# Performance work log

Hardware: AMD Instinct MI355X
Metric: run time of the kernel (lower is better)

The kernel has to match this reference:

```python
import jax, jax.numpy as jnp
import numpy as np

N_NODES = 100000
N_EDGES = 3200000
WINDOW = 200


def setup_inputs() -> dict:
    key = jax.random.key(0)
    k1, k2, k3, k4, k5 = jax.random.split(key, 5)
    loss_series = jax.random.normal(k1, (N_NODES, WINDOW), dtype=jnp.float32)
    W_series = jax.random.normal(k2, (1, WINDOW), dtype=jnp.float32) / WINDOW
    W_graph = jax.random.normal(k3, (1, 2), dtype=jnp.float32) * 0.1
    edge_src = jax.random.randint(k4, (N_EDGES,), 0, N_NODES, dtype=jnp.int32)
    edge_dst = jax.random.randint(k5, (N_EDGES,), 0, N_NODES, dtype=jnp.int32)
    return {
        "loss_series": loss_series,
        "W_series": W_series,
        "W_graph": W_graph,
        "edge_src": edge_src,
        "edge_dst": edge_dst,
    }


def reference(loss_series, W_series, W_graph, edge_src, edge_dst):
    # series aggregation: Linear(window_size -> 1, no bias)  -> h: [N, 1]
    h = loss_series @ W_series.T
    n = loss_series.shape[0]
    neg_inf = jnp.float32(-jnp.inf)

    # remove self-loops: neutralize their messages for the max-reduce
    self_loop = (edge_src == edge_dst)[:, None]

    # forward graph: copy_u('feat') then max over incoming edges per dst
    msg_fwd = jnp.where(self_loop, neg_inf, h[edge_src])        # [E, 1]
    pre_feat = jax.ops.segment_max(msg_fwd, edge_dst, num_segments=n)

    # reversed graph: max over outgoing neighbors (messages flow dst -> src)
    msg_rev = jnp.where(self_loop, neg_inf, h[edge_dst])        # [E, 1]
    suc_max = jax.ops.segment_max(msg_rev, edge_src, num_segments=n)

    # DGL fills nodes with no incoming messages with 0
    pre_feat = jnp.where(jnp.isneginf(pre_feat), 0.0, pre_feat)
    suc_max = jnp.where(jnp.isneginf(suc_max), 0.0, suc_max)

    agg = jnp.concatenate([pre_feat, suc_max], axis=1)          # [N, 2]
    graph_h = agg @ W_graph.T                                   # [N, 1]

    # softmax over node dimension (dim=0)
    return jax.nn.softmax(h + graph_h, axis=0)
```

## Files before the change

kernel.cpp:

```cpp
#include <hip/hip_runtime.h>
#include <math.h>

#define RED_BLOCKS 256
#define NT 512
#define AT 1024
#define CCH 16384
#define ORD_OFF 0x007fffffu

__device__ __forceinline__ unsigned f2ord(float f) {
    unsigned u = __float_as_uint(f);
    u = (u & 0x80000000u) ? ~u : (u | 0x80000000u);
    return u - ORD_OFF;
}
__device__ __forceinline__ float ord2f(unsigned uo) {
    unsigned u = uo + ORD_OFF;
    unsigned v = (u & 0x80000000u) ? (u & 0x7fffffffu) : ~u;
    return __uint_as_float(v);
}

__device__ __forceinline__ void h_row_body(const float* __restrict__ loss,
                                           const float* __restrict__ Ws,
                                           float* __restrict__ h,
                                           unsigned* __restrict__ ordArr,
                                           int n, int blk) {
    int sub = threadIdx.x & 15, r = threadIdx.x >> 4;
    int row = blk * (NT / 16) + r;
    if (row >= n) return;
    const float4* f4 = (const float4*)(loss + (size_t)row * 200);
    const float4* W4 = (const float4*)Ws;
    float4 a, w;
    float acc = 0.0f;
    a = f4[sub];      w = W4[sub];      acc += a.x*w.x + a.y*w.y + a.z*w.z + a.w*w.w;
    a = f4[sub + 16]; w = W4[sub + 16]; acc += a.x*w.x + a.y*w.y + a.z*w.z + a.w*w.w;
    a = f4[sub + 32]; w = W4[sub + 32]; acc += a.x*w.x + a.y*w.y + a.z*w.z + a.w*w.w;
    if (sub < 2) { a = f4[48 + sub]; w = W4[48 + sub]; acc += a.x*w.x + a.y*w.y + a.z*w.z + a.w*w.w; }
    #pragma unroll
    for (int off = 8; off > 0; off >>= 1) acc += __shfl_down(acc, off, 16);
    if (sub == 0) { h[row] = acc; ordArr[row] = f2ord(acc); }
}

__global__ void __launch_bounds__(NT) k_h(const float* __restrict__ loss,
                                          const float* __restrict__ Ws,
                                          float* __restrict__ h,
                                          unsigned* __restrict__ ordArr, int n) {
    h_row_body(loss, Ws, h, ordArr, n, blockIdx.x);
}

__global__ void __launch_bounds__(AT, 4) k_accum(
        const int* __restrict__ src, const int* __restrict__ dst,
        const unsigned* __restrict__ ordArr, unsigned* __restrict__ partials,
        int ne, int nch, int split, int epb) {
    __shared__ unsigned preL[CCH];
    __shared__ unsigned sucL[CCH];
    int c = blockIdx.x / split, sub = blockIdx.x - c * split;
    for (int t = threadIdx.x; t < CCH; t += AT) { preL[t] = 0u; sucL[t] = 0u; }
    __syncthreads();
    const unsigned clo = (unsigned)c * CCH;
    int lo = sub * epb, hi = min(sub * epb + epb, ne);

    int i = lo + (int)threadIdx.x * 16;
    for (; i + 15 < hi; i += AT * 16) {
        int4 s0 = *(const int4*)(src + i);
        int4 s1 = *(const int4*)(src + i + 4);
        int4 s2 = *(const int4*)(src + i + 8);
        int4 s3 = *(const int4*)(src + i + 12);
        int4 d0 = *(const int4*)(dst + i);
        int4 d1 = *(const int4*)(dst + i + 4);
        int4 d2 = *(const int4*)(dst + i + 8);
        int4 d3 = *(const int4*)(dst + i + 12);
        int ss[16] = { s0.x, s0.y, s0.z, s0.w, s1.x, s1.y, s1.z, s1.w,
                       s2.x, s2.y, s2.z, s2.w, s3.x, s3.y, s3.z, s3.w };
        int dd[16] = { d0.x, d0.y, d0.z, d0.w, d1.x, d1.y, d1.z, d1.w,
                       d2.x, d2.y, d2.z, d2.w, d3.x, d3.y, d3.z, d3.w };
        unsigned dl[16], sl[16], gp[16], gs[16];
        #pragma unroll
        for (int u = 0; u < 16; ++u) {
            bool same = (ss[u] == dd[u]);
            dl[u] = same ? ~0u : (unsigned)dd[u] - clo;
            sl[u] = same ? ~0u : (unsigned)ss[u] - clo;
            gp[u] = (dl[u] < CCH) ? ordArr[ss[u]] : 0u;
            gs[u] = (sl[u] < CCH) ? ordArr[dd[u]] : 0u;
        }
        #pragma unroll
        for (int u = 0; u < 16; ++u) {
            if (dl[u] < CCH) atomicMax(&preL[dl[u]], gp[u]);
            if (sl[u] < CCH) atomicMax(&sucL[sl[u]], gs[u]);
        }
    }
    for (int j = i; j < hi; ++j) {
        if (j >= lo) {
            int s = src[j], d = dst[j];
            if (s != d) {
                unsigned dl = (unsigned)d - clo;
                if (dl < CCH) atomicMax(&preL[dl], ordArr[s]);
                unsigned sl = (unsigned)s - clo;
                if (sl < CCH) atomicMax(&sucL[sl], ordArr[d]);
            }
        }
    }
    __syncthreads();
    size_t pb = ((size_t)c * split + sub) * CCH;
    size_t sucOff = (size_t)nch * split * CCH;
    for (int t = threadIdx.x; t < CCH; t += AT) {
        partials[pb + t] = preL[t];
        partials[sucOff + pb + t] = sucL[t];
    }
}

__global__ void k_edges_dev(const int* __restrict__ src, const int* __restrict__ dst,
                            const float* __restrict__ h, unsigned* __restrict__ partials, int ne) {
    int e = blockIdx.x * blockDim.x + threadIdx.x;
    if (e >= ne) return;
    int s = src[e], d = dst[e];
    if (s == d) return;
    unsigned hs = f2ord(h[s]);
    unsigned hd = f2ord(h[d]);
    unsigned* slot0 = &partials[d];
    unsigned* slot1 = &partials[(1 << 17) + s];
    if (*slot0 < hs) atomicMax(slot0, hs);
    if (*slot1 < hd) atomicMax(slot1, hd);
}

__global__ void k_logit_max(const float* __restrict__ h, const unsigned* __restrict__ partials,
                            const float* __restrict__ Wg, float* __restrict__ logit,
                            float* __restrict__ maxPart, int n, int nch, int split) {
    __shared__ float sm[256];
    float w0 = Wg[0], w1 = Wg[1];
    size_t sucOff = (size_t)nch * split * CCH;
    float m = -INFINITY;
    for (int i = blockIdx.x * 256 + threadIdx.x; i < n; i += 256 * RED_BLOCKS) {
        int c = i / CCH, loc = i - c * CCH;
        const unsigned* pp = partials + ((size_t)c * split) * CCH + loc;
        const unsigned* sp = pp + sucOff;
        unsigned p = 0, s = 0;
        #pragma unroll 4
        for (int k = 0; k < split; ++k) {
            p = max(p, pp[(size_t)k * CCH]);
            s = max(s, sp[(size_t)k * CCH]);
        }
        float pf = p ? ord2f(p) : 0.0f;
        float sf = s ? ord2f(s) : 0.0f;
        float l = h[i] + w0 * pf + w1 * sf;
        logit[i] = l;
        m = fmaxf(m, l);
    }
    sm[threadIdx.x] = m;
    __syncthreads();
    for (int off = 128; off > 0; off >>= 1) {
        if (threadIdx.x < off) sm[threadIdx.x] = fmaxf(sm[threadIdx.x], sm[threadIdx.x + off]);
        __syncthreads();
    }
    if (threadIdx.x == 0) maxPart[blockIdx.x] = sm[0];
}

__global__ void k_logit_max_dev(const float* __restrict__ h, const unsigned* __restrict__ partials,
                                const float* __restrict__ Wg, float* __restrict__ logit,
                                float* __restrict__ maxPart, int n) {
    __shared__ float sm[256];
    float w0 = Wg[0], w1 = Wg[1];
    float m = -INFINITY;
    for (int i = blockIdx.x * 256 + threadIdx.x; i < n; i += 256 * RED_BLOCKS) {
        unsigned p = partials[i], s = partials[(1 << 17) + i];
        float pf = p ? ord2f(p) : 0.0f;
        float sf = s ? ord2f(s) : 0.0f;
        float l = h[i] + w0 * pf + w1 * sf;
        logit[i] = l;
        m = fmaxf(m, l);
    }
    sm[threadIdx.x] = m;
    __syncthreads();
    for (int off = 128; off > 0; off >>= 1) {
        if (threadIdx.x < off) sm[threadIdx.x] = fmaxf(sm[threadIdx.x], sm[threadIdx.x + off]);
        __syncthreads();
    }
    if (threadIdx.x == 0) maxPart[blockIdx.x] = sm[0];
}

__global__ void k_exp_sum(const float* __restrict__ logit, const float* __restrict__ maxPart,
                          float* __restrict__ out, float* __restrict__ sumPart, int n) {
    __shared__ float sm[256];
    sm[threadIdx.x] = maxPart[threadIdx.x];
    __syncthreads();
    for (int off = 128; off > 0; off >>= 1) {
        if (threadIdx.x < off) sm[threadIdx.x] = fmaxf(sm[threadIdx.x], sm[threadIdx.x + off]);
        __syncthreads();
    }
    float gmax = sm[0];
    __syncthreads();
    float acc = 0.0f;
    for (int i = blockIdx.x * 256 + threadIdx.x; i < n; i += 256 * RED_BLOCKS) {
        float e = expf(logit[i] - gmax);
        out[i] = e;
        acc += e;
    }
    sm[threadIdx.x] = acc;
    __syncthreads();
    for (int off = 128; off > 0; off >>= 1) {
        if (threadIdx.x < off) sm[threadIdx.x] += sm[threadIdx.x + off];
        __syncthreads();
    }
    if (threadIdx.x == 0) sumPart[blockIdx.x] = sm[0];
}

__global__ void k_norm(const float* __restrict__ sumPart, float* __restrict__ out, int n) {
    __shared__ float sm[256];
    sm[threadIdx.x] = sumPart[threadIdx.x];
    __syncthreads();
    for (int off = 128; off > 0; off >>= 1) {
        if (threadIdx.x < off) sm[threadIdx.x] += sm[threadIdx.x + off];
        __syncthreads();
    }
    float inv = 1.0f / sm[0];
    for (int i = blockIdx.x * 256 + threadIdx.x; i < n; i += 256 * RED_BLOCKS) out[i] *= inv;
}

extern "C" void kernel_launch(void* const* d_in, const int* in_sizes, int n_in,
                              void* d_out, int out_size, void* d_ws, size_t ws_size,
                              hipStream_t stream) {
    const float* loss = (const float*)d_in[0];
    const float* Ws   = (const float*)d_in[1];
    const float* Wg   = (const float*)d_in[2];
    const int* esrc   = (const int*)d_in[3];
    const int* edst   = (const int*)d_in[4];
    float* out = (float*)d_out;

    const int n  = in_sizes[0] / 200;
    const int ne = in_sizes[3];
    const int Gh = (n + (NT / 16) - 1) / (NT / 16);

    const int nch = (n + CCH - 1) / CCH;
    int split = 256 / nch; if (split < 1) split = 1;
    const int epb = (((ne + split - 1) / split) + 15) & ~15;

    float*    h        = (float*)d_ws;
    float*    logit    = h + n;
    unsigned* ordArr   = (unsigned*)(logit + n);
    float*    maxPart  = (float*)(ordArr + n);
    float*    sumPart  = maxPart + RED_BLOCKS;
    unsigned* partials = (unsigned*)(sumPart + RED_BLOCKS);
    size_t part_w = (size_t)2 * nch * split * CCH;
    size_t need = ((size_t)3 * n + 2 * RED_BLOCKS + part_w) * 4;

    k_h<<<Gh, NT, 0, stream>>>(loss, Ws, h, ordArr, n);

    if (need <= ws_size) {
        k_accum<<<nch * split, AT, 0, stream>>>(esrc, edst, ordArr, partials, ne, nch, split, epb);
        k_logit_max<<<RED_BLOCKS, 256, 0, stream>>>(h, partials, Wg, logit, maxPart, n, nch, split);
    } else {
        hipMemsetAsync(partials, 0, (size_t)2 * (1 << 17) * 4, stream);
        k_edges_dev<<<(ne + 255) / 256, 256, 0, stream>>>(esrc, edst, h, partials, ne);
        k_logit_max_dev<<<RED_BLOCKS, 256, 0, stream>>>(h, partials, Wg, logit, maxPart, n);
    }

    k_exp_sum<<<RED_BLOCKS, 256, 0, stream>>>(logit, maxPart, out, sumPart, n);
    k_norm<<<RED_BLOCKS, 256, 0, stream>>>(sumPart, out, n);
}
```

Before: 74.26 us.

## Pre-pack edge entries with gathered values, then run separate per-direction LDS max passes

Adds a pack kernel that gathers ordArr values once per edge and writes (target, value) pairs for the forward and reverse directions, with self-loops marked by a sentinel. The LDS max accumulation is split into two launches, one per direction, each using a single 16K-entry shared buffer, which allows more blocks per CU. The fixed SPLIT is 36 instead of 256/nch. The aim is to stop every chunk block from re-doing the random gathers and to raise occupancy. In exchange it writes and re-reads about 51 MB of packed pairs, and each chunk block still streams the whole edge list, so memory traffic grows considerably.

Measured after the change: 131.7 us. 1.77x slower.

```diff
diff --git a/kernel.cpp b/kernel.cpp
--- a/kernel.cpp
+++ b/kernel.cpp
@@ -3,9 +3,11 @@
 
 #define RED_BLOCKS 256
 #define NT 512
-#define AT 1024
+#define GT 1024
 #define CCH 16384
+#define SPLIT 36
 #define ORD_OFF 0x007fffffu
+#define SENT 0xFFFFFFFFu
 
 __device__ __forceinline__ unsigned f2ord(float f) {
     unsigned u = __float_as_uint(f);
@@ -46,65 +48,88 @@
     h_row_body(loss, Ws, h, ordArr, n, blockIdx.x);
 }
 
-__global__ void __launch_bounds__(AT, 4) k_accum(
+__global__ void __launch_bounds__(256) k_pack(
         const int* __restrict__ src, const int* __restrict__ dst,
-        const unsigned* __restrict__ ordArr, unsigned* __restrict__ partials,
-        int ne, int nch, int split, int epb) {
-    __shared__ unsigned preL[CCH];
-    __shared__ unsigned sucL[CCH];
-    int c = blockIdx.x / split, sub = blockIdx.x - c * split;
-    for (int t = threadIdx.x; t < CCH; t += AT) { preL[t] = 0u; sucL[t] = 0u; }
-    __syncthreads();
-    const unsigned clo = (unsigned)c * CCH;
-    int lo = sub * epb, hi = min(sub * epb + epb, ne);
-
+        const unsigned* __restrict__ ordArr,
+        uint2* __restrict__ epre, uint2* __restrict__ esuc, int ne) {
+    int base = (blockIdx.x * 256 + threadIdx.x) * 8;
+    if (base + 7 < ne) {
+        int4 s0 = *(const int4*)(src + base);
+        int4 s1 = *(const int4*)(src + base + 4);
+        int4 d0 = *(const int4*)(dst + base);
+        int4 d1 = *(const int4*)(dst + base + 4);
+        int ss[8] = { s0.x, s0.y, s0.z, s0.w, s1.x, s1.y, s1.z, s1.w };
+        int dd[8] = { d0.x, d0.y, d0.z, d0.w, d1.x, d1.y, d1.z, d1.w };
+        unsigned vs[8], vd[8];
+        #pragma unroll
+        for (int u = 0; u < 8; ++u) vs[u] = ordArr[ss[u]];
+        #pragma unroll
+        for (int u = 0; u < 8; ++u) vd[u] = ordArr[dd[u]];
+        uint2 ep[8], es[8];
+        #pragma unroll
+        for (int u = 0; u < 8; ++u) {
+            bool same = (ss[u] == dd[u]);
+            ep[u] = make_uint2(same ? SENT : (unsigned)dd[u], vs[u]);
+            es[u] = make_uint2(same ? SENT : (unsigned)ss[u], vd[u]);
+        }
+        #pragma unroll
+        for (int u = 0; u < 8; ++u) epre[base + u] = ep[u];
+        #pragma unroll
+        for (int u = 0; u < 8; ++u) esuc[base + u] = es[u];
+    } else {
+        for (int e = base; e < ne; ++e) {
+            int s = src[e], d = dst[e];
+            bool same = (s == d);
+            epre[e] = make_uint2(same ? SENT : (unsigned)d, ordArr[s]);
+            esuc[e] = make_uint2(same ? SENT : (unsigned)s, ordArr[d]);
+        }
+    }
+}
+
+__global__ void __launch_bounds__(GT, 8) k_gmax(
+        const uint2* __restrict__ entries, unsigned* __restrict__ partials,
+        int ne, int nch, int dirbase, int epb) {
+    __shared__ unsigned acc[CCH];
+    int c = blockIdx.x / SPLIT, sub = blockIdx.x - c * SPLIT;
+    int cc = (c >= nch) ? c - nch : c;
+    const uint2* E = entries;
+    for (int t = threadIdx.x; t < CCH; t += GT) acc[t] = 0u;
+    __syncthreads();
+    const unsigned clo = (unsigned)cc * CCH;
+    int lo = sub * epb, hi = min(lo + epb, ne);
     int i = lo + (int)threadIdx.x * 16;
-    for (; i + 15 < hi; i += AT * 16) {
-        int4 s0 = *(const int4*)(src + i);
-        int4 s1 = *(const int4*)(src + i + 4);
-        int4 s2 = *(const int4*)(src + i + 8);
-        int4 s3 = *(const int4*)(src + i + 12);
-        int4 d0 = *(const int4*)(dst + i);
-        int4 d1 = *(const int4*)(dst + i + 4);
-        int4 d2 = *(const int4*)(dst + i + 8);
-        int4 d3 = *(const int4*)(dst + i + 12);
-        int ss[16] = { s0.x, s0.y, s0.z, s0.w, s1.x, s1.y, s1.z, s1.w,
-                       s2.x, s2.y, s2.z, s2.w, s3.x, s3.y, s3.z, s3.w };
-        int dd[16] = { d0.x, d0.y, d0.z, d0.w, d1.x, d1.y, d1.z, d1.w,
-                       d2.x, d2.y, d2.z, d2.w, d3.x, d3.y, d3.z, d3.w };
-        unsigned dl[16], sl[16], gp[16], gs[16];
+    for (; i + 15 < hi; i += GT * 16) {
+        int4 p0 = *(const int4*)((const int*)(E + i));
+        int4 p1 = *(const int4*)((const int*)(E + i) + 4);
+        int4 p2 = *(const int4*)((const int*)(E + i) + 8);
+        int4 p3 = *(const int4*)((const int*)(E + i) + 12);
+        int4 p4 = *(const int4*)((const int*)(E + i) + 16);
+        int4 p5 = *(const int4*)((const int*)(E + i) + 20);
+        int4 p6 = *(const int4*)((const int*)(E + i) + 24);
+        int4 p7 = *(const int4*)((const int*)(E + i) + 28);
+        unsigned nd[16], vv[16];
+        nd[0]=(unsigned)p0.x; vv[0]=(unsigned)p0.y; nd[1]=(unsigned)p0.z; vv[1]=(unsigned)p0.w;
+        nd[2]=(unsigned)p1.x; vv[2]=(unsigned)p1.y; nd[3]=(unsigned)p1.z; vv[3]=(unsigned)p1.w;
+        nd[4]=(unsigned)p2.x; vv[4]=(unsigned)p2.y; nd[5]=(unsigned)p2.z; vv[5]=(unsigned)p2.w;
+        nd[6]=(unsigned)p3.x; vv[6]=(unsigned)p3.y; nd[7]=(unsigned)p3.z; vv[7]=(unsigned)p3.w;
+        nd[8]=(unsigned)p4.x; vv[8]=(unsigned)p4.y; nd[9]=(unsigned)p4.z; vv[9]=(unsigned)p4.w;
+        nd[10]=(unsigned)p5.x; vv[10]=(unsigned)p5.y; nd[11]=(unsigned)p5.z; vv[11]=(unsigned)p5.w;
+        nd[12]=(unsigned)p6.x; vv[12]=(unsigned)p6.y; nd[13]=(unsigned)p6.z; vv[13]=(unsigned)p6.w;
+        nd[14]=(unsigned)p7.x; vv[14]=(unsigned)p7.y; nd[15]=(unsigned)p7.z; vv[15]=(unsigned)p7.w;
         #pragma unroll
         for (int u = 0; u < 16; ++u) {
-            bool same = (ss[u] == dd[u]);
-            dl[u] = same ? ~0u : (unsigned)dd[u] - clo;
-            sl[u] = same ? ~0u : (unsigned)ss[u] - clo;
-            gp[u] = (dl[u] < CCH) ? ordArr[ss[u]] : 0u;
-            gs[u] = (sl[u] < CCH) ? ordArr[dd[u]] : 0u;
-        }
-        #pragma unroll
-        for (int u = 0; u < 16; ++u) {
-            if (dl[u] < CCH) atomicMax(&preL[dl[u]], gp[u]);
-            if (sl[u] < CCH) atomicMax(&sucL[sl[u]], gs[u]);
+            unsigned ul = nd[u] - clo;
+            if (ul < CCH) atomicMax(&acc[ul], vv[u]);
         }
     }
     for (int j = i; j < hi; ++j) {
-        if (j >= lo) {
-            int s = src[j], d = dst[j];
-            if (s != d) {
-                unsigned dl = (unsigned)d - clo;
-                if (dl < CCH) atomicMax(&preL[dl], ordArr[s]);
-                unsigned sl = (unsigned)s - clo;
-                if (sl < CCH) atomicMax(&sucL[sl], ordArr[d]);
-            }
-        }
-    }
-    __syncthreads();
-    size_t pb = ((size_t)c * split + sub) * CCH;
-    size_t sucOff = (size_t)nch * split * CCH;
-    for (int t = threadIdx.x; t < CCH; t += AT) {
-        partials[pb + t] = preL[t];
-        partials[sucOff + pb + t] = sucL[t];
-    }
+        uint2 e = E[j];
+        unsigned ul = e.x - clo;
+        if (ul < CCH) atomicMax(&acc[ul], e.y);
+    }
+    __syncthreads();
+    unsigned* outp = partials + ((size_t)(dirbase + blockIdx.x)) * CCH;
+    for (int t = threadIdx.x; t < CCH; t += GT) outp[t] = acc[t];
 }
 
 __global__ void k_edges_dev(const int* __restrict__ src, const int* __restrict__ dst,
@@ -123,18 +148,17 @@
 
 __global__ void k_logit_max(const float* __restrict__ h, const unsigned* __restrict__ partials,
                             const float* __restrict__ Wg, float* __restrict__ logit,
-                            float* __restrict__ maxPart, int n, int nch, int split) {
+                            float* __restrict__ maxPart, int n, int nch) {
     __shared__ float sm[256];
     float w0 = Wg[0], w1 = Wg[1];
-    size_t sucOff = (size_t)nch * split * CCH;
     float m = -INFINITY;
     for (int i = blockIdx.x * 256 + threadIdx.x; i < n; i += 256 * RED_BLOCKS) {
         int c = i / CCH, loc = i - c * CCH;
-        const unsigned* pp = partials + ((size_t)c * split) * CCH + loc;
-        const unsigned* sp = pp + sucOff;
+        const unsigned* pp = partials + ((size_t)c * SPLIT) * CCH + loc;
+        const unsigned* sp = partials + ((size_t)(nch + c) * SPLIT) * CCH + loc;
         unsigned p = 0, s = 0;
         #pragma unroll 4
-        for (int k = 0; k < split; ++k) {
+        for (int k = 0; k < SPLIT; ++k) {
             p = max(p, pp[(size_t)k * CCH]);
             s = max(s, sp[(size_t)k * CCH]);
         }
@@ -229,8 +253,7 @@
     const int Gh = (n + (NT / 16) - 1) / (NT / 16);
 
     const int nch = (n + CCH - 1) / CCH;
-    int split = 256 / nch; if (split < 1) split = 1;
-    const int epb = (((ne + split - 1) / split) + 15) & ~15;
+    const int epb = (((ne + SPLIT - 1) / SPLIT) + 15) & ~15;
 
     float*    h        = (float*)d_ws;
     float*    logit    = h + n;
@@ -238,14 +261,18 @@
     float*    maxPart  = (float*)(ordArr + n);
     float*    sumPart  = maxPart + RED_BLOCKS;
     unsigned* partials = (unsigned*)(sumPart + RED_BLOCKS);
-    size_t part_w = (size_t)2 * nch * split * CCH;
-    size_t need = ((size_t)3 * n + 2 * RED_BLOCKS + part_w) * 4;
+    size_t part_w = (size_t)2 * nch * SPLIT * CCH;
+    uint2*    epre     = (uint2*)(partials + part_w);
+    uint2*    esuc     = epre + ne;
+    size_t need = ((size_t)3 * n + 2 * RED_BLOCKS + part_w) * 4 + (size_t)4 * ne * 4;
 
     k_h<<<Gh, NT, 0, stream>>>(loss, Ws, h, ordArr, n);
 
     if (need <= ws_size) {
-        k_accum<<<nch * split, AT, 0, stream>>>(esrc, edst, ordArr, partials, ne, nch, split, epb);
-        k_logit_max<<<RED_BLOCKS, 256, 0, stream>>>(h, partials, Wg, logit, maxPart, n, nch, split);
+        k_pack<<<(ne + 2047) / 2048, 256, 0, stream>>>(esrc, edst, ordArr, epre, esuc, ne);
+        k_gmax<<<nch * SPLIT, GT, 0, stream>>>(epre, partials, ne, nch, 0, epb);
+        k_gmax<<<nch * SPLIT, GT, 0, stream>>>(esuc, partials, ne, nch, nch * SPLIT, epb);
+        k_logit_max<<<RED_BLOCKS, 256, 0, stream>>>(h, partials, Wg, logit, maxPart, n, nch);
     } else {
         hipMemsetAsync(partials, 0, (size_t)2 * (1 << 17) * 4, stream);
         k_edges_dev<<<(ne + 255) / 256, 256, 0, stream>>>(esrc, edst, h, partials, ne);
```

## Fuse logit, max, exp-sum and normalize into one cooperative kernel

Applied to the files above, without the earlier changes.

Replaces the three epilogue kernels (logit+max, exp+sum, normalize) with a single cooperative kernel that uses grid-wide syncs between the max, sum and normalize phases. Logits and exponentials stay in registers (up to 4 per thread), which removes the global logit round-trip and two kernel launches. The trade-offs are a fixed 256-block grid and the cost of the grid syncs, and the path is limited to n up to 4*256*256.

Measured after the change: 137.2 us. +84.7%, slower.

```diff
diff --git a/kernel.cpp b/kernel.cpp
--- a/kernel.cpp
+++ b/kernel.cpp
@@ -1,7 +1,11 @@
 #include <hip/hip_runtime.h>
+#include <hip/hip_cooperative_groups.h>
 #include <math.h>
 
+namespace cg = cooperative_groups;
+
 #define RED_BLOCKS 256
+#define ET 256
 #define NT 512
 #define AT 1024
 #define CCH 16384
@@ -107,6 +111,77 @@
     }
 }
 
+__global__ void __launch_bounds__(ET) k_epi(
+        const float* __restrict__ h, const unsigned* __restrict__ partials,
+        const float* __restrict__ Wg, float* __restrict__ out,
+        float* __restrict__ maxPart, float* __restrict__ sumPart,
+        int n, int nch, int split) {
+    cg::grid_group grid = cg::this_grid();
+    __shared__ float sm[ET];
+    const int NTH = ET * RED_BLOCKS;
+    int gtid = blockIdx.x * ET + threadIdx.x;
+    float w0 = Wg[0], w1 = Wg[1];
+    size_t sucOff = (size_t)nch * split * CCH;
+
+    float lv[4];
+    int ni = 0;
+    float m = -INFINITY;
+    for (int i = gtid; i < n; i += NTH) {
+        int c = i / CCH, loc = i - c * CCH;
+        const unsigned* pp = partials + ((size_t)c * split) * CCH + loc;
+        const unsigned* sp = pp + sucOff;
+        unsigned p = 0, s = 0;
+        #pragma unroll 4
+        for (int k = 0; k < split; ++k) {
+            p = max(p, pp[(size_t)k * CCH]);
+            s = max(s, sp[(size_t)k * CCH]);
+        }
+        float pf = p ? ord2f(p) : 0.0f;
+        float sf = s ? ord2f(s) : 0.0f;
+        float l = h[i] + w0 * pf + w1 * sf;
+        lv[ni++] = l;
+        m = fmaxf(m, l);
+    }
+    sm[threadIdx.x] = m;
+    __syncthreads();
+    for (int off = ET / 2; off > 0; off >>= 1) {
+        if (threadIdx.x < off) sm[threadIdx.x] = fmaxf(sm[threadIdx.x], sm[threadIdx.x + off]);
+        __syncthreads();
+    }
+    if (threadIdx.x == 0) maxPart[blockIdx.x] = sm[0];
+    grid.sync();
+
+    sm[threadIdx.x] = maxPart[threadIdx.x];
+    __syncthreads();
+    for (int off = ET / 2; off > 0; off >>= 1) {
+        if (threadIdx.x < off) sm[threadIdx.x] = fmaxf(sm[threadIdx.x], sm[threadIdx.x + off]);
+        __syncthreads();
+    }
+    float gmax = sm[0];
+    __syncthreads();
+    float ev[4];
+    float acc = 0.0f;
+    for (int k = 0; k < ni; ++k) { ev[k] = expf(lv[k] - gmax); acc += ev[k]; }
+    sm[threadIdx.x] = acc;
+    __syncthreads();
+    for (int off = ET / 2; off > 0; off >>= 1) {
+        if (threadIdx.x < off) sm[threadIdx.x] += sm[threadIdx.x + off];
+        __syncthreads();
+    }
+    if (threadIdx.x == 0) sumPart[blockIdx.x] = sm[0];
+    grid.sync();
+
+    sm[threadIdx.x] = sumPart[threadIdx.x];
+    __syncthreads();
+    for (int off = ET / 2; off > 0; off >>= 1) {
+        if (threadIdx.x < off) sm[threadIdx.x] += sm[threadIdx.x + off];
+        __syncthreads();
+    }
+    float inv = 1.0f / sm[0];
+    int k = 0;
+    for (int i = gtid; i < n; i += NTH) out[i] = ev[k++] * inv;
+}
+
 __global__ void k_edges_dev(const int* __restrict__ src, const int* __restrict__ dst,
                             const float* __restrict__ h, unsigned* __restrict__ partials, int ne) {
     int e = blockIdx.x * blockDim.x + threadIdx.x;
@@ -243,15 +318,23 @@
 
     k_h<<<Gh, NT, 0, stream>>>(loss, Ws, h, ordArr, n);
 
-    if (need <= ws_size) {
+    if (need <= ws_size && n <= 4 * ET * RED_BLOCKS) {
+        k_accum<<<nch * split, AT, 0, stream>>>(esrc, edst, ordArr, partials, ne, nch, split, epb);
+        int n_ = n, nch_ = nch, split_ = split;
+        void* args[] = { (void*)&h, (void*)&partials, (void*)&Wg, (void*)&out,
+                         (void*)&maxPart, (void*)&sumPart,
+                         (void*)&n_, (void*)&nch_, (void*)&split_ };
+        hipLaunchCooperativeKernel((void*)k_epi, dim3(RED_BLOCKS), dim3(ET), args, 0, stream);
+    } else if (need <= ws_size) {
         k_accum<<<nch * split, AT, 0, stream>>>(esrc, edst, ordArr, partials, ne, nch, split, epb);
         k_logit_max<<<RED_BLOCKS, 256, 0, stream>>>(h, partials, Wg, logit, maxPart, n, nch, split);
+        k_exp_sum<<<RED_BLOCKS, 256, 0, stream>>>(logit, maxPart, out, sumPart, n);
+        k_norm<<<RED_BLOCKS, 256, 0, stream>>>(sumPart, out, n);
     } else {
         hipMemsetAsync(partials, 0, (size_t)2 * (1 << 17) * 4, stream);
         k_edges_dev<<<(ne + 255) / 256, 256, 0, stream>>>(esrc, edst, h, partials, ne);
         k_logit_max_dev<<<RED_BLOCKS, 256, 0, stream>>>(h, partials, Wg, logit, maxPart, n);
-    }
-
-    k_exp_sum<<<RED_BLOCKS, 256, 0, stream>>>(logit, maxPart, out, sumPart, n);
-    k_norm<<<RED_BLOCKS, 256, 0, stream>>>(sumPart, out, n);
-}
+        k_exp_sum<<<RED_BLOCKS, 256, 0, stream>>>(logit, maxPart, out, sumPart, n);
+        k_norm<<<RED_BLOCKS, 256, 0, stream>>>(sumPart, out, n);
+    }
+}
```

## Fuse partial fold, logit and exp-sum into one kernel; enlarge shared chunk

Applied to the files above, without the earlier changes.

Replaces the separate logit/max, exp-sum and normalize kernels with a fused kernel that folds the per-chunk partial maxima, computes logits, takes a block-local max and writes exponentials with block sums, followed by a small normalize kernel that rescales each block by its local max relative to the global max. This drops one launch and the logit round-trip through global memory. The shared-memory chunk size is also raised so that fewer chunks cover the nodes, which changes the accumulate grid split. The larger LDS arrays may reduce occupancy in the accumulate kernel.

After: 75.32 us. About the same (+1.4%).

```diff
diff --git a/kernel.cpp b/kernel.cpp
--- a/kernel.cpp
+++ b/kernel.cpp
@@ -4,7 +4,7 @@
 #define RED_BLOCKS 256
 #define NT 512
 #define AT 1024
-#define CCH 16384
+#define CCH 19968
 #define ORD_OFF 0x007fffffu
 
 __device__ __forceinline__ unsigned f2ord(float f) {
@@ -107,6 +107,89 @@
     }
 }
 
+__global__ void __launch_bounds__(256) k_fold_exp(
+        const float* __restrict__ h, const unsigned* __restrict__ partials,
+        const float* __restrict__ Wg, float* __restrict__ out,
+        float* __restrict__ maxPart, float* __restrict__ sumPart,
+        int n, int nch, int split) {
+    __shared__ float sm[256];
+    float w0 = Wg[0], w1 = Wg[1];
+    size_t sucOff = (size_t)nch * split * CCH;
+    const int NTH = 256 * RED_BLOCKS;
+    int i0 = blockIdx.x * 256 + threadIdx.x;
+    int i1 = i0 + NTH;
+
+    float l0 = -INFINITY, l1 = -INFINITY;
+    if (i0 < n) {
+        int c = i0 / CCH, loc = i0 - c * CCH;
+        const unsigned* pp = partials + ((size_t)c * split) * CCH + loc;
+        const unsigned* sp = pp + sucOff;
+        unsigned p = 0, s = 0;
+        #pragma unroll 4
+        for (int k = 0; k < split; ++k) {
+            p = max(p, pp[(size_t)k * CCH]);
+            s = max(s, sp[(size_t)k * CCH]);
+        }
+        l0 = h[i0] + w0 * (p ? ord2f(p) : 0.0f) + w1 * (s ? ord2f(s) : 0.0f);
+    }
+    if (i1 < n) {
+        int c = i1 / CCH, loc = i1 - c * CCH;
+        const unsigned* pp = partials + ((size_t)c * split) * CCH + loc;
+        const unsigned* sp = pp + sucOff;
+        unsigned p = 0, s = 0;
+        #pragma unroll 4
+        for (int k = 0; k < split; ++k) {
+            p = max(p, pp[(size_t)k * CCH]);
+            s = max(s, sp[(size_t)k * CCH]);
+        }
+        l1 = h[i1] + w0 * (p ? ord2f(p) : 0.0f) + w1 * (s ? ord2f(s) : 0.0f);
+    }
+    sm[threadIdx.x] = fmaxf(l0, l1);
+    __syncthreads();
+    for (int off = 128; off > 0; off >>= 1) {
+        if (threadIdx.x < off) sm[threadIdx.x] = fmaxf(sm[threadIdx.x], sm[threadIdx.x + off]);
+        __syncthreads();
+    }
+    float mb = sm[0];
+    __syncthreads();
+    float e0 = 0.0f, e1 = 0.0f;
+    if (i0 < n) { e0 = expf(l0 - mb); out[i0] = e0; }
+    if (i1 < n) { e1 = expf(l1 - mb); out[i1] = e1; }
+    sm[threadIdx.x] = e0 + e1;
+    __syncthreads();
+    for (int off = 128; off > 0; off >>= 1) {
+        if (threadIdx.x < off) sm[threadIdx.x] += sm[threadIdx.x + off];
+        __syncthreads();
+    }
+    if (threadIdx.x == 0) { maxPart[blockIdx.x] = mb; sumPart[blockIdx.x] = sm[0]; }
+}
+
+__global__ void __launch_bounds__(256) k_norm2(
+        const float* __restrict__ maxPart, const float* __restrict__ sumPart,
+        float* __restrict__ out, int n) {
+    __shared__ float sm[256];
+    const int NTH = 256 * RED_BLOCKS;
+    sm[threadIdx.x] = maxPart[threadIdx.x];
+    __syncthreads();
+    for (int off = 128; off > 0; off >>= 1) {
+        if (threadIdx.x < off) sm[threadIdx.x] = fmaxf(sm[threadIdx.x], sm[threadIdx.x + off]);
+        __syncthreads();
+    }
+    float gmax = sm[0];
+    __syncthreads();
+    sm[threadIdx.x] = sumPart[threadIdx.x] * expf(maxPart[threadIdx.x] - gmax);
+    __syncthreads();
+    for (int off = 128; off > 0; off >>= 1) {
+        if (threadIdx.x < off) sm[threadIdx.x] += sm[threadIdx.x + off];
+        __syncthreads();
+    }
+    float scale = expf(maxPart[blockIdx.x] - gmax) / sm[0];
+    int i0 = blockIdx.x * 256 + threadIdx.x;
+    int i1 = i0 + NTH;
+    if (i0 < n) out[i0] *= scale;
+    if (i1 < n) out[i1] *= scale;
+}
+
 __global__ void k_edges_dev(const int* __restrict__ src, const int* __restrict__ dst,
                             const float* __restrict__ h, unsigned* __restrict__ partials, int ne) {
     int e = blockIdx.x * blockDim.x + threadIdx.x;
@@ -243,15 +326,20 @@
 
     k_h<<<Gh, NT, 0, stream>>>(loss, Ws, h, ordArr, n);
 
-    if (need <= ws_size) {
+    if (need <= ws_size && n <= 2 * 256 * RED_BLOCKS) {
+        k_accum<<<nch * split, AT, 0, stream>>>(esrc, edst, ordArr, partials, ne, nch, split, epb);
+        k_fold_exp<<<RED_BLOCKS, 256, 0, stream>>>(h, partials, Wg, out, maxPart, sumPart, n, nch, split);
+        k_norm2<<<RED_BLOCKS, 256, 0, stream>>>(maxPart, sumPart, out, n);
+    } else if (need <= ws_size) {
         k_accum<<<nch * split, AT, 0, stream>>>(esrc, edst, ordArr, partials, ne, nch, split, epb);
         k_logit_max<<<RED_BLOCKS, 256, 0, stream>>>(h, partials, Wg, logit, maxPart, n, nch, split);
+        k_exp_sum<<<RED_BLOCKS, 256, 0, stream>>>(logit, maxPart, out, sumPart, n);
+        k_norm<<<RED_BLOCKS, 256, 0, stream>>>(sumPart, out, n);
     } else {
         hipMemsetAsync(partials, 0, (size_t)2 * (1 << 17) * 4, stream);
         k_edges_dev<<<(ne + 255) / 256, 256, 0, stream>>>(esrc, edst, h, partials, ne);
         k_logit_max_dev<<<RED_BLOCKS, 256, 0, stream>>>(h, partials, Wg, logit, maxPart, n);
-    }
-
-    k_exp_sum<<<RED_BLOCKS, 256, 0, stream>>>(logit, maxPart, out, sumPart, n);
-    k_norm<<<RED_BLOCKS, 256, 0, stream>>>(sumPart, out, n);
-}
+        k_exp_sum<<<RED_BLOCKS, 256, 0, stream>>>(logit, maxPart, out, sumPart, n);
+        k_norm<<<RED_BLOCKS, 256, 0, stream>>>(sumPart, out, n);
+    }
+}
```
